# Kernel tuning notes

Hardware: AMD Instinct MI355X
Metric: run time of the kernel (lower is better)

## Reference

```python
import jax, jax.numpy as jnp
import numpy as np

N_NODES = 10000


def setup_inputs() -> dict:
    key = jax.random.key(0)
    ks = jax.random.split(key, 12)
    B, N, H, D_IN, E = 8, N_NODES, 128, 256, 160000
    s = 0.05
    return {
        "x": jax.random.normal(ks[0], (B, D_IN), jnp.float32),
        "h_prev": jax.random.normal(ks[1], (B, N, H), jnp.float32),
        "src": jax.random.randint(ks[2], (E,), 0, N, jnp.int32),
        "dst": jax.random.randint(ks[3], (E,), 0, N, jnp.int32),
        "w_r": jax.random.normal(ks[4], (D_IN, H), jnp.float32) * s,
        "b_r": jax.random.normal(ks[5], (H,), jnp.float32) * s,
        "w_z": jax.random.normal(ks[6], (D_IN, H), jnp.float32) * s,
        "b_z": jax.random.normal(ks[7], (H,), jnp.float32) * s,
        "w_h": jax.random.normal(ks[8], (D_IN, H), jnp.float32) * s,
        "b_h": jax.random.normal(ks[9], (H,), jnp.float32) * s,
        "gcn_w": jax.random.normal(ks[10], (H, H), jnp.float32) * s,
        "gcn_b": jax.random.normal(ks[11], (H,), jnp.float32) * s,
    }


def _graph_conv(h, src, dst, gcn_w, gcn_b):
    """DGL GraphConv, norm='both': out = D_in^{-1/2} A D_out^{-1/2} h W + b.
    h: (B, N, H); same graph structure shared across the batch."""
    N = h.shape[1]
    ones = jnp.ones(src.shape, h.dtype)
    out_deg = jax.ops.segment_sum(ones, src, num_segments=N)
    in_deg = jax.ops.segment_sum(ones, dst, num_segments=N)
    norm_out = jnp.where(out_deg > 0, jax.lax.rsqrt(jnp.maximum(out_deg, 1.0)), 0.0)
    norm_in = jnp.where(in_deg > 0, jax.lax.rsqrt(jnp.maximum(in_deg, 1.0)), 0.0)
    hs = h * norm_out[None, :, None]            # (B, N, H)
    msg = hs[:, src, :]                          # (B, E, H) gather
    agg = jax.vmap(lambda m: jax.ops.segment_sum(m, dst, num_segments=N))(msg)
    agg = agg * norm_in[None, :, None]
    return jnp.einsum('bnh,hk->bnk', agg, gcn_w) + gcn_b


def reference(x, h_prev, src, dst, w_r, b_r, w_z, b_z, w_h, b_h, gcn_w, gcn_b):
    h_conv = _graph_conv(h_prev, src, dst, gcn_w, gcn_b)   # (B, N, H)
    x_r = (x @ w_r + b_r)[:, None, :]                      # (B, 1, H) broadcast over N
    x_z = (x @ w_z + b_z)[:, None, :]
    x_h = (x @ w_h + b_h)[:, None, :]
    r_t = jax.nn.sigmoid(x_r + h_conv)
    z_t = jax.nn.sigmoid(x_z + h_conv)
    h_tilde = jnp.tanh(x_h + r_t * h_conv)
    return (1.0 - z_t) * h_prev + z_t * h_tilde
```

## Files before the change

kernel.cpp:

```cpp
#include <hip/hip_runtime.h>
#include <hip/hip_bf16.h>

#define B_   8
#define N_   10000
#define H_   128
#define DIN_ 256
#define E_   160000
#define EPAD_ (E_ + 7 * N_ + 8)

typedef unsigned int uint_;
typedef unsigned short ushort_;
typedef __attribute__((ext_vector_type(8))) short short8;
typedef __attribute__((ext_vector_type(4))) float f32x4;

__device__ __forceinline__ float sigmoidf_(float v) { return 1.f / (1.f + __expf(-v)); }
__device__ __forceinline__ float tanh_fast(float v) { float e = __expf(2.f * v); return 1.f - 2.f / (e + 1.f); }

__device__ __forceinline__ ushort_ f2bf(float f) {
    union { float f; uint_ u; } v; v.f = f;
    uint_ r = v.u + 0x7fff + ((v.u >> 16) & 1);
    return (ushort_)(r >> 16);
}
#define BF_LO(u) __uint_as_float((u) << 16)
#define BF_HI(u) __uint_as_float((u) & 0xffff0000u)

__global__ __launch_bounds__(256) void degrees_k(const int* __restrict__ src, const int* __restrict__ dst,
                                                 int* __restrict__ out_deg, int* __restrict__ in_deg) {
    int e = blockIdx.x * 256 + threadIdx.x;
    if (e < E_) {
        atomicAdd(&out_deg[src[e]], 1);
        atomicAdd(&in_deg[dst[e]], 1);
    }
}

__global__ __launch_bounds__(1024) void norms_scan_k(const int* __restrict__ out_deg, const int* __restrict__ in_deg,
                                                     float* __restrict__ norm_out, float* __restrict__ norm_in,
                                                     int* __restrict__ offsets) {
    __shared__ int buf[10240];
    __shared__ int part[1024];
    const int tid = threadIdx.x;
    #pragma unroll
    for (int q = 0; q < 10; ++q) {
        int idx = q * 1024 + tid;
        int d = (idx < N_) ? in_deg[idx] : 0;
        buf[idx] = (idx < N_) ? ((d + 7) & ~7) : 0;
        if (idx < N_) {
            int od = out_deg[idx];
            norm_out[idx] = od > 0 ? rsqrtf((float)od) : 0.f;
            norm_in[idx]  = d  > 0 ? rsqrtf((float)d)  : 0.f;
        }
    }
    __syncthreads();
    int local[10];
    int s = 0;
    #pragma unroll
    for (int q = 0; q < 10; ++q) {
        local[q] = s;
        s += buf[tid * 10 + q];
    }
    part[tid] = s;
    __syncthreads();
    for (int off = 1; off < 1024; off <<= 1) {
        int v = (tid >= off) ? part[tid - off] : 0;
        __syncthreads();
        part[tid] += v;
        __syncthreads();
    }
    int pre = (tid > 0) ? part[tid - 1] : 0;
    #pragma unroll
    for (int q = 0; q < 10; ++q)
        buf[tid * 10 + q] = pre + local[q];
    __syncthreads();
    #pragma unroll
    for (int q = 0; q < 10; ++q) {
        int idx = q * 1024 + tid;
        if (idx < N_) offsets[idx] = buf[idx];
    }
    if (tid == 1023) offsets[N_] = part[1023];
}

__global__ __launch_bounds__(256) void fill_csr_k(const int* __restrict__ src, const int* __restrict__ dst,
                                                  const int* __restrict__ offsets, int* __restrict__ cursor,
                                                  const float* __restrict__ norm_out,
                                                  int2* __restrict__ csr_ed) {
    int e = blockIdx.x * 256 + threadIdx.x;
    if (e < E_) {
        int d = dst[e];
        int s = src[e];
        int pos = offsets[d] + atomicAdd(&cursor[d], 1);
        csr_ed[pos] = make_int2(s, __float_as_int(norm_out[s]));
    }
}

__global__ __launch_bounds__(256) void xproj_k(const float* __restrict__ x,
                                               const float* __restrict__ w_r, const float* __restrict__ b_r,
                                               const float* __restrict__ w_z, const float* __restrict__ b_z,
                                               const float* __restrict__ w_h, const float* __restrict__ b_h,
                                               const float* __restrict__ gcn_w, ushort_* __restrict__ wt,
                                               float* __restrict__ xr, float* __restrict__ xz, float* __restrict__ xh) {
    const int g = blockIdx.x, b = blockIdx.y;
    if (g == 3) {
        if (b != 0) return;
        const int t = threadIdx.x;
        const int n = t >> 1;
        const int kb = (t & 1) * 64;
        #pragma unroll
        for (int i = 0; i < 8; ++i) {
            int k = kb + i * 8;
            uint4 o;
            o.x = (uint_)f2bf(gcn_w[(k + 0) * H_ + n]) | ((uint_)f2bf(gcn_w[(k + 1) * H_ + n]) << 16);
            o.y = (uint_)f2bf(gcn_w[(k + 2) * H_ + n]) | ((uint_)f2bf(gcn_w[(k + 3) * H_ + n]) << 16);
            o.z = (uint_)f2bf(gcn_w[(k + 4) * H_ + n]) | ((uint_)f2bf(gcn_w[(k + 5) * H_ + n]) << 16);
            o.w = (uint_)f2bf(gcn_w[(k + 6) * H_ + n]) | ((uint_)f2bf(gcn_w[(k + 7) * H_ + n]) << 16);
            *(uint4*)(wt + n * H_ + k) = o;
        }
        return;
    }
    const float* __restrict__ w  = g == 0 ? w_r : (g == 1 ? w_z : w_h);
    const float* __restrict__ bs = g == 0 ? b_r : (g == 1 ? b_z : b_h);
    float* __restrict__ o        = g == 0 ? xr  : (g == 1 ? xz  : xh);
    const int k = threadIdx.x & 127, half = threadIdx.x >> 7;
    const float* xb = x + b * DIN_;
    float a = 0.f;
    #pragma unroll 8
    for (int d = half * 128; d < half * 128 + 128; ++d)
        a += xb[d] * w[d * H_ + k];
    __shared__ float part[2][128];
    part[half][k] = a;
    __syncthreads();
    if (half == 0) o[b * H_ + k] = a + part[1][k] + bs[k];
}

__global__ __launch_bounds__(256) void gemm_cast_k(const float* __restrict__ h,
                                                   const ushort_* __restrict__ wt,
                                                   ushort_* __restrict__ hw) {
    __shared__ ushort_ WT_s[H_ * H_];
    __shared__ ushort_ A_s[64 * H_];
    const int tid = threadIdx.x;
    const int b = blockIdx.x;
    const size_t bslab = (size_t)b * N_;

    #pragma unroll
    for (int i = 0; i < 8; ++i) {
        int c = i * 256 + tid;
        int n = c >> 4;
        int kus = (c & 15) * 8;
        uint4 v = ((const uint4*)wt)[c];
        *(uint4*)&WT_s[n * H_ + (kus ^ ((n & 7) << 3))] = v;
    }

    const int l = tid & 63;
    const int w = tid >> 6;
    const int lr = l & 15;
    const int kg = (l >> 4) * 8;
    const int arow = w * 16 + lr;

    for (int t = blockIdx.y; t < 157; t += 79) {
        const int n0 = t * 64;
        #pragma unroll
        for (int i = 0; i < 8; ++i) {
            int f4 = i * 256 + tid;
            int row = f4 >> 5;
            int col4 = (f4 & 31) * 4;
            f32x4 v = {0.f, 0.f, 0.f, 0.f};
            if (n0 + row < N_) v = *(const f32x4*)&h[(bslab + n0 + row) * H_ + col4];
            uint2 p;
            p.x = (uint_)f2bf(v[0]) | ((uint_)f2bf(v[1]) << 16);
            p.y = (uint_)f2bf(v[2]) | ((uint_)f2bf(v[3]) << 16);
            *(uint2*)&A_s[row * H_ + (col4 ^ ((row & 7) << 3))] = p;
        }
        __syncthreads();

        f32x4 acc[8];
        #pragma unroll
        for (int nf = 0; nf < 8; ++nf) acc[nf] = (f32x4){0.f, 0.f, 0.f, 0.f};

        #pragma unroll
        for (int kk = 0; kk < 4; ++kk) {
            int kus = kk * 32 + kg;
            short8 av = *(const short8*)&A_s[arow * H_ + (kus ^ ((arow & 7) << 3))];
            #pragma unroll
            for (int nf = 0; nf < 8; ++nf) {
                int nrow = nf * 16 + lr;
                short8 bv = *(const short8*)&WT_s[nrow * H_ + (kus ^ ((nrow & 7) << 3))];
                acc[nf] = __builtin_amdgcn_mfma_f32_16x16x32_bf16(av, bv, acc[nf], 0, 0, 0);
            }
        }

        const int wrow0 = w * 16 + (l >> 4) * 4;
        #pragma unroll
        for (int nf = 0; nf < 8; ++nf) {
            int col = nf * 16 + lr;
            #pragma unroll
            for (int r = 0; r < 4; ++r) {
                int row = wrow0 + r;
                A_s[row * H_ + (col ^ ((row & 7) << 3))] = f2bf(acc[nf][r]);
            }
        }
        __syncthreads();
        {
            int row = w * 16 + (l >> 2);
            int c0 = (l & 3) * 32;
            int swz = (row & 7) << 3;
            if (n0 + row < N_) {
                uint4 o0 = *(const uint4*)&A_s[row * H_ + ((c0 +  0) ^ swz)];
                uint4 o1 = *(const uint4*)&A_s[row * H_ + ((c0 +  8) ^ swz)];
                uint4 o2 = *(const uint4*)&A_s[row * H_ + ((c0 + 16) ^ swz)];
                uint4 o3 = *(const uint4*)&A_s[row * H_ + ((c0 + 24) ^ swz)];
                uint4* dst = (uint4*)(hw + (bslab + n0 + row) * (size_t)H_ + c0);
                dst[0] = o0; dst[1] = o1; dst[2] = o2; dst[3] = o3;
            }
        }
        __syncthreads();
    }
}

__global__ __launch_bounds__(256) void agg_gru_k(const ushort_* __restrict__ hw, const int* __restrict__ offsets,
                                                 const float* __restrict__ norm_in,
                                                 const int2* __restrict__ csr_ed,
                                                 const float* __restrict__ gcn_b,
                                                 const float* __restrict__ xr, const float* __restrict__ xz,
                                                 const float* __restrict__ xh,
                                                 const float* __restrict__ h_prev, float* __restrict__ out) {
    const int lane = threadIdx.x & 63;
    const int wave = threadIdx.x >> 6;
    const int b  = blockIdx.x & 7;
    const int ng = blockIdx.x >> 3;
    const int n  = ng * 4 + wave;
    const int o  = __builtin_amdgcn_readfirstlane(offsets[n]);
    const int dc = __builtin_amdgcn_readfirstlane(offsets[n + 1]) - o;
    const int2* __restrict__ ed = csr_ed + o;
    const ushort_* __restrict__ hb = hw + (size_t)b * (N_ * H_) + lane * 2;

    const float ni = norm_in[n];
    const int col = lane * 2;
    const size_t off = ((size_t)b * N_ + n) * H_ + col;
    float2 hp = *(const float2*)(h_prev + off);
    float2 gb = *(const float2*)(gcn_b + col);
    float2 vr = *(const float2*)(xr + b * H_ + col);
    float2 vz = *(const float2*)(xz + b * H_ + col);
    float2 vh = *(const float2*)(xh + b * H_ + col);

    float a0 = 0.f, a1 = 0.f;
    for (int j = 0; j < dc; j += 8) {
        #pragma unroll
        for (int q = 0; q < 8; ++q) {
            int2 eq = ed[j + q];
            int   s = __builtin_amdgcn_readfirstlane(eq.x);
            float c = __uint_as_float((uint_)eq.y);
            uint_ u = *(const uint_*)(hb + (size_t)s * H_);
            a0 += c * BF_LO(u);
            a1 += c * BF_HI(u);
        }
    }

    float2 wv;
    {
        float hc = a0 * ni + gb.x;
        float rr = sigmoidf_(vr.x + hc);
        float zz = sigmoidf_(vz.x + hc);
        float ht = tanh_fast(vh.x + rr * hc);
        wv.x = (1.f - zz) * hp.x + zz * ht;
    }
    {
        float hc = a1 * ni + gb.y;
        float rr = sigmoidf_(vr.y + hc);
        float zz = sigmoidf_(vz.y + hc);
        float ht = tanh_fast(vh.y + rr * hc);
        wv.y = (1.f - zz) * hp.y + zz * ht;
    }
    *(float2*)(out + off) = wv;
}

extern "C" void kernel_launch(void* const* d_in, const int* in_sizes, int n_in,
                              void* d_out, int out_size, void* d_ws, size_t ws_size,
                              hipStream_t stream) {
    (void)in_sizes; (void)n_in; (void)out_size; (void)ws_size;
    const float* x      = (const float*)d_in[0];
    const float* h_prev = (const float*)d_in[1];
    const int*   src    = (const int*)d_in[2];
    const int*   dst    = (const int*)d_in[3];
    const float* w_r    = (const float*)d_in[4];
    const float* b_r    = (const float*)d_in[5];
    const float* w_z    = (const float*)d_in[6];
    const float* b_z    = (const float*)d_in[7];
    const float* w_h    = (const float*)d_in[8];
    const float* b_h    = (const float*)d_in[9];
    const float* gcn_w  = (const float*)d_in[10];
    const float* gcn_b  = (const float*)d_in[11];
    float* out = (float*)d_out;

    ushort_* hw = (ushort_*)d_ws;
    int* wsi = (int*)(hw + (size_t)B_ * N_ * H_);
    int* out_deg   = wsi;
    int* in_deg    = wsi + N_;
    int* cursor    = wsi + 2 * N_;
    int2* csr_ed   = (int2*)(wsi + 3 * N_);
    int* offsets   = (int*)(csr_ed + EPAD_);
    float* norm_out = (float*)(offsets + N_ + 1);
    float* norm_in  = norm_out + N_;
    float* xr = norm_in + N_;
    float* xz = xr + B_ * H_;
    float* xh = xz + B_ * H_;
    ushort_* wt = (ushort_*)(xh + B_ * H_);

    hipMemsetAsync(out_deg, 0, 3 * N_ * sizeof(int) + EPAD_ * sizeof(int2), stream);
    degrees_k<<<(E_ + 255) / 256, 256, 0, stream>>>(src, dst, out_deg, in_deg);
    norms_scan_k<<<1, 1024, 0, stream>>>(out_deg, in_deg, norm_out, norm_in, offsets);
    fill_csr_k<<<(E_ + 255) / 256, 256, 0, stream>>>(src, dst, offsets, cursor, norm_out, csr_ed);
    xproj_k<<<dim3(4, B_), 256, 0, stream>>>(x, w_r, b_r, w_z, b_z, w_h, b_h, gcn_w, wt, xr, xz, xh);
    gemm_cast_k<<<dim3(8, 79), 256, 0, stream>>>(h_prev, wt, hw);
    agg_gru_k<<<(N_ / 4) * 8, 256, 0, stream>>>(hw, offsets, norm_in, csr_ed,
                                                gcn_b, xr, xz, xh, h_prev, out);
}
```

Measured before the change: 114.3 us.

## Hold GEMM weights in registers with 512-thread blocks; prefetch CSR edges in aggregation

The GEMM-cast kernel moves to 512 threads, with 8 waves split into row groups and column halves. Each wave now keeps its slice of the transposed weight matrix in registers instead of loading it into shared memory, and the output goes through a separate C_s buffer. This removes the 32KB shared-memory weight staging and its per-tile LDS reads, at the cost of more register pressure. The aggregation kernel software-pipelines the edge-list loads, fetching the next 8 edges while it processes the current 8, so edge-index latency is hidden behind the gather.

```diff
diff --git a/kernel.cpp b/kernel.cpp
--- a/kernel.cpp
+++ b/kernel.cpp
@@ -131,35 +131,35 @@
     if (half == 0) o[b * H_ + k] = a + part[1][k] + bs[k];
 }
 
-__global__ __launch_bounds__(256) void gemm_cast_k(const float* __restrict__ h,
-                                                   const ushort_* __restrict__ wt,
-                                                   ushort_* __restrict__ hw) {
-    __shared__ ushort_ WT_s[H_ * H_];
+__global__ __launch_bounds__(512, 3) void gemm_cast_k(const float* __restrict__ h,
+                                                      const ushort_* __restrict__ wt,
+                                                      ushort_* __restrict__ hw) {
     __shared__ ushort_ A_s[64 * H_];
+    __shared__ ushort_ C_s[64 * H_];
     const int tid = threadIdx.x;
     const int b = blockIdx.x;
     const size_t bslab = (size_t)b * N_;
 
-    #pragma unroll
-    for (int i = 0; i < 8; ++i) {
-        int c = i * 256 + tid;
-        int n = c >> 4;
-        int kus = (c & 15) * 8;
-        uint4 v = ((const uint4*)wt)[c];
-        *(uint4*)&WT_s[n * H_ + (kus ^ ((n & 7) << 3))] = v;
-    }
-
-    const int l = tid & 63;
-    const int w = tid >> 6;
+    const int l  = tid & 63;
+    const int w  = tid >> 6;
+    const int rg = w >> 1;
+    const int ch = w & 1;
     const int lr = l & 15;
     const int kg = (l >> 4) * 8;
-    const int arow = w * 16 + lr;
+    const int arow = rg * 16 + lr;
+
+    short8 breg[4][4];
+    #pragma unroll
+    for (int kk = 0; kk < 4; ++kk)
+        #pragma unroll
+        for (int nf = 0; nf < 4; ++nf)
+            breg[kk][nf] = *(const short8*)&wt[(ch * 64 + nf * 16 + lr) * H_ + kk * 32 + kg];
 
     for (int t = blockIdx.y; t < 157; t += 79) {
         const int n0 = t * 64;
         #pragma unroll
-        for (int i = 0; i < 8; ++i) {
-            int f4 = i * 256 + tid;
+        for (int i = 0; i < 4; ++i) {
+            int f4 = i * 512 + tid;
             int row = f4 >> 5;
             int col4 = (f4 & 31) * 4;
             f32x4 v = {0.f, 0.f, 0.f, 0.f};
@@ -171,49 +171,53 @@
         }
         __syncthreads();
 
-        f32x4 acc[8];
-        #pragma unroll
-        for (int nf = 0; nf < 8; ++nf) acc[nf] = (f32x4){0.f, 0.f, 0.f, 0.f};
+        f32x4 acc[4];
+        #pragma unroll
+        for (int nf = 0; nf < 4; ++nf) acc[nf] = (f32x4){0.f, 0.f, 0.f, 0.f};
 
         #pragma unroll
         for (int kk = 0; kk < 4; ++kk) {
             int kus = kk * 32 + kg;
             short8 av = *(const short8*)&A_s[arow * H_ + (kus ^ ((arow & 7) << 3))];
             #pragma unroll
-            for (int nf = 0; nf < 8; ++nf) {
-                int nrow = nf * 16 + lr;
-                short8 bv = *(const short8*)&WT_s[nrow * H_ + (kus ^ ((nrow & 7) << 3))];
-                acc[nf] = __builtin_amdgcn_mfma_f32_16x16x32_bf16(av, bv, acc[nf], 0, 0, 0);
-            }
-        }
-
-        const int wrow0 = w * 16 + (l >> 4) * 4;
-        #pragma unroll
-        for (int nf = 0; nf < 8; ++nf) {
-            int col = nf * 16 + lr;
+            for (int nf = 0; nf < 4; ++nf)
+                acc[nf] = __builtin_amdgcn_mfma_f32_16x16x32_bf16(av, breg[kk][nf], acc[nf], 0, 0, 0);
+        }
+
+        const int wrow0 = rg * 16 + (l >> 4) * 4;
+        #pragma unroll
+        for (int nf = 0; nf < 4; ++nf) {
+            int col = ch * 64 + nf * 16 + lr;
             #pragma unroll
             for (int r = 0; r < 4; ++r) {
                 int row = wrow0 + r;
-                A_s[row * H_ + (col ^ ((row & 7) << 3))] = f2bf(acc[nf][r]);
+                C_s[row * H_ + (col ^ ((row & 7) << 3))] = f2bf(acc[nf][r]);
             }
         }
         __syncthreads();
         {
-            int row = w * 16 + (l >> 2);
-            int c0 = (l & 3) * 32;
+            int row = tid >> 3;
+            int c0 = (tid & 7) * 16;
             int swz = (row & 7) << 3;
             if (n0 + row < N_) {
-                uint4 o0 = *(const uint4*)&A_s[row * H_ + ((c0 +  0) ^ swz)];
-                uint4 o1 = *(const uint4*)&A_s[row * H_ + ((c0 +  8) ^ swz)];
-                uint4 o2 = *(const uint4*)&A_s[row * H_ + ((c0 + 16) ^ swz)];
-                uint4 o3 = *(const uint4*)&A_s[row * H_ + ((c0 + 24) ^ swz)];
+                uint4 o0 = *(const uint4*)&C_s[row * H_ + ((c0 + 0) ^ swz)];
+                uint4 o1 = *(const uint4*)&C_s[row * H_ + ((c0 + 8) ^ swz)];
                 uint4* dst = (uint4*)(hw + (bslab + n0 + row) * (size_t)H_ + c0);
-                dst[0] = o0; dst[1] = o1; dst[2] = o2; dst[3] = o3;
+                dst[0] = o0; dst[1] = o1;
             }
         }
         __syncthreads();
     }
 }
+
+#define PROC_(E)                                                  \
+    {                                                             \
+        int   s_ = __builtin_amdgcn_readfirstlane((E).x);         \
+        float c_ = __uint_as_float((uint_)(E).y);                 \
+        uint_ u_ = *(const uint_*)(hb + (size_t)s_ * H_);         \
+        a0 += c_ * BF_LO(u_);                                     \
+        a1 += c_ * BF_HI(u_);                                     \
+    }
 
 __global__ __launch_bounds__(256) void agg_gru_k(const ushort_* __restrict__ hw, const int* __restrict__ offsets,
                                                  const float* __restrict__ norm_in,
@@ -242,16 +246,19 @@
     float2 vh = *(const float2*)(xh + b * H_ + col);
 
     float a0 = 0.f, a1 = 0.f;
-    for (int j = 0; j < dc; j += 8) {
-        #pragma unroll
-        for (int q = 0; q < 8; ++q) {
-            int2 eq = ed[j + q];
-            int   s = __builtin_amdgcn_readfirstlane(eq.x);
-            float c = __uint_as_float((uint_)eq.y);
-            uint_ u = *(const uint_*)(hb + (size_t)s * H_);
-            a0 += c * BF_LO(u);
-            a1 += c * BF_HI(u);
-        }
+    if (dc > 0) {
+        int2 c0 = ed[0], c1 = ed[1], c2 = ed[2], c3 = ed[3];
+        int2 c4 = ed[4], c5 = ed[5], c6 = ed[6], c7 = ed[7];
+        for (int j = 8; j < dc; j += 8) {
+            int2 p0 = ed[j + 0], p1 = ed[j + 1], p2 = ed[j + 2], p3 = ed[j + 3];
+            int2 p4 = ed[j + 4], p5 = ed[j + 5], p6 = ed[j + 6], p7 = ed[j + 7];
+            PROC_(c0); PROC_(c1); PROC_(c2); PROC_(c3);
+            PROC_(c4); PROC_(c5); PROC_(c6); PROC_(c7);
+            c0 = p0; c1 = p1; c2 = p2; c3 = p3;
+            c4 = p4; c5 = p5; c6 = p6; c7 = p7;
+        }
+        PROC_(c0); PROC_(c1); PROC_(c2); PROC_(c3);
+        PROC_(c4); PROC_(c5); PROC_(c6); PROC_(c7);
     }
 
     float2 wv;
@@ -309,7 +316,7 @@
     norms_scan_k<<<1, 1024, 0, stream>>>(out_deg, in_deg, norm_out, norm_in, offsets);
     fill_csr_k<<<(E_ + 255) / 256, 256, 0, stream>>>(src, dst, offsets, cursor, norm_out, csr_ed);
     xproj_k<<<dim3(4, B_), 256, 0, stream>>>(x, w_r, b_r, w_z, b_z, w_h, b_h, gcn_w, wt, xr, xz, xh);
-    gemm_cast_k<<<dim3(8, 79), 256, 0, stream>>>(h_prev, wt, hw);
+    gemm_cast_k<<<dim3(8, 79), 512, 0, stream>>>(h_prev, wt, hw);
     agg_gru_k<<<(N_ / 4) * 8, 256, 0, stream>>>(hw, offsets, norm_in, csr_ed,
                                                 gcn_b, xr, xz, xh, h_prev, out);
 }
```

Measured after the change: 121.6 us. 6.4% more time.
